# Kernel tuning notes

Measured on AMD Instinct MI355X. Metric: run time of the kernel, lower is better.

The kernel has to match this reference:

```python
import jax, jax.numpy as jnp
import numpy as np

N = 100000   # nodes
E = 1600000  # edges
D = 128      # feature dim (layers all 128)
G = 512      # graphs in batch
C = 10       # num_classes
EPS = 1e-5   # batchnorm eps


def setup_inputs() -> dict:
    key = jax.random.key(0)
    ks = jax.random.split(key, 16)
    s = 1.0 / np.sqrt(D)
    return {
        "x": jax.random.normal(ks[0], (N, D), jnp.float32),
        "edge_index": jax.random.randint(ks[1], (2, E), 0, N),
        "batch": jnp.sort(jax.random.randint(ks[2], (N,), 0, G)),
        "w1": jax.random.normal(ks[3], (D, D), jnp.float32) * s,
        "b1": jnp.zeros((D,), jnp.float32),
        "w2": jax.random.normal(ks[4], (D, D), jnp.float32) * s,
        "b2": jnp.zeros((D,), jnp.float32),
        "w3": jax.random.normal(ks[5], (D, D), jnp.float32) * s,
        "b3": jnp.zeros((D,), jnp.float32),
        "g1": jnp.ones((D,), jnp.float32),
        "be1": jnp.zeros((D,), jnp.float32),
        "g2": jnp.ones((D,), jnp.float32),
        "be2": jnp.zeros((D,), jnp.float32),
        "fc_w": jax.random.normal(ks[6], (D, C), jnp.float32) * s,
        "fc_b": jnp.zeros((C,), jnp.float32),
    }


def _gcn(x, src, dst, norm, W, b):
    # transform -> gather -> normalize -> scatter-add (PyG GCNConv)
    h = x @ W
    out = jax.ops.segment_sum(h[src] * norm[:, None], dst, num_segments=x.shape[0])
    return out + b


def _bn(x, g, b):
    # training-mode BatchNorm1d: batch mean / biased variance
    mu = jnp.mean(x, axis=0)
    var = jnp.mean((x - mu) ** 2, axis=0)
    return (x - mu) * jax.lax.rsqrt(var + EPS) * g + b


def reference(x, edge_index, batch, w1, b1, w2, b2, w3, b3, g1, be1, g2, be2, fc_w, fc_b):
    n = x.shape[0]
    loop = jnp.arange(n)
    src = jnp.concatenate([edge_index[0], loop])  # add self-loops
    dst = jnp.concatenate([edge_index[1], loop])
    deg = jax.ops.segment_sum(jnp.ones_like(src, x.dtype), dst, num_segments=n)
    dinv = jax.lax.rsqrt(jnp.maximum(deg, 1.0))  # deg >= 1 due to self-loops
    norm = dinv[src] * dinv[dst]  # symmetric normalization per edge

    h = jax.nn.relu(_gcn(x, src, dst, norm, w1, b1))        # conv1 + relu (bn1 unused, per source)
    h = jax.nn.relu(_gcn(h, src, dst, norm, w2, b2))        # conv2 + relu
    h = jax.nn.relu(_bn(h, g1, be1))                        # bn + relu
    h = jax.nn.relu(_gcn(h, src, dst, norm, w3, b3))        # conv3 + relu
    h = jax.nn.relu(_bn(h, g2, be2))                        # bn + relu

    cnt = jax.ops.segment_sum(jnp.ones((n,), h.dtype), batch, num_segments=G)
    pooled = jax.ops.segment_sum(h, batch, num_segments=G) / jnp.maximum(cnt, 1.0)[:, None]
    logits = pooled @ fc_w + fc_b
    return jax.nn.log_softmax(logits, axis=1)
```

## Files before the change

### kernel.cpp

```cpp
#include <hip/hip_runtime.h>
#include <hip/hip_bf16.h>
#include <math.h>

#define D 128
#define G_GRAPHS 512
#define C_CLASSES 10
#define BN_EPS 1e-5f
#define NBUCK_MAX 512
#define EDGE_CHUNK 4096
#define EPT 16

typedef unsigned short u16;
typedef unsigned int u32;
typedef unsigned short ushort4_t __attribute__((ext_vector_type(4)));
typedef unsigned short ushort8_t __attribute__((ext_vector_type(8)));
typedef __bf16 bf16x8 __attribute__((ext_vector_type(8)));
typedef float floatx4 __attribute__((ext_vector_type(4)));
union B8 { ushort8_t u; bf16x8 b; };

__device__ __forceinline__ float bf_lo(u32 v) { return __uint_as_float(v << 16); }
__device__ __forceinline__ float bf_hi(u32 v) { return __uint_as_float(v & 0xffff0000u); }
__device__ __forceinline__ u16 f2bf(float f) {
    union { float f; u32 u; } x; x.f = f;
    u32 r = x.u + 0x7fff + ((x.u >> 16) & 1);
    return (u16)(r >> 16);
}
__device__ __forceinline__ u32 pack2bf(float a, float b) {
    return (u32)f2bf(a) | ((u32)f2bf(b) << 16);
}


__global__ __launch_bounds__(256) void bucket_hist_kernel(
    const int* __restrict__ dst, int* __restrict__ bucketCnt, int E, int nbuck)
{
    __shared__ int h[NBUCK_MAX];
    int tid = threadIdx.x;
    for (int i = tid; i < NBUCK_MAX; i += 256) h[i] = 0;
    __syncthreads();
    for (int i = blockIdx.x * 256 + tid; i < E; i += gridDim.x * 256)
        atomicAdd(&h[dst[i] >> 8], 1);
    __syncthreads();
    for (int i = tid; i < nbuck; i += 256)
        if (h[i]) atomicAdd(&bucketCnt[i], h[i]);
}

__global__ void scan_buckets_kernel(
    const int* __restrict__ bucketCnt, int* __restrict__ bucketBase,
    int* __restrict__ bucketCursor, int* __restrict__ rowPtr, int nbuck, int N, int E)
{
    __shared__ int buf[2][512];
    int tid = threadIdx.x;
    int v = (tid < nbuck) ? bucketCnt[tid] : 0;
    buf[0][tid] = v;
    __syncthreads();
    int cur = 0;
    for (int off = 1; off < 512; off <<= 1) {
        buf[1 - cur][tid] = buf[cur][tid] + ((tid >= off) ? buf[cur][tid - off] : 0);
        cur ^= 1;
        __syncthreads();
    }
    if (tid < nbuck) {
        int b = buf[cur][tid] - v;
        bucketBase[tid] = b;
        bucketCursor[tid] = b;
    }
    if (tid == 0) { bucketBase[nbuck] = E; rowPtr[N] = E; }
}

__global__ __launch_bounds__(256) void scatter_pairs_kernel(
    const int* __restrict__ src, const int* __restrict__ dst,
    int* __restrict__ bucketCursor, u32* __restrict__ pairs, int E)
{
    __shared__ int h[NBUCK_MAX];
    __shared__ int base[NBUCK_MAX];
    int tid = threadIdx.x;
    int e0 = blockIdx.x * EDGE_CHUNK;
    for (int i = tid; i < NBUCK_MAX; i += 256) h[i] = 0;
    __syncthreads();
    int s[EPT], d[EPT], r[EPT];
#pragma unroll
    for (int j = 0; j < EPT; ++j) {
        int i = e0 + j * 256 + tid;
        if (i < E) {
            s[j] = src[i];
            d[j] = dst[i];
            r[j] = atomicAdd(&h[d[j] >> 8], 1);
        } else {
            d[j] = -1;
        }
    }
    __syncthreads();
    for (int i = tid; i < NBUCK_MAX; i += 256)
        if (h[i]) base[i] = atomicAdd(&bucketCursor[i], h[i]);
    __syncthreads();
#pragma unroll
    for (int j = 0; j < EPT; ++j) {
        if (d[j] >= 0) {
            int b = d[j] >> 8;
            pairs[base[b] + r[j]] = ((u32)s[j] << 8) | (u32)(d[j] & 255);
        }
    }
}

__global__ __launch_bounds__(256) void bucket_sort_kernel(
    const u32* __restrict__ pairs, const int* __restrict__ bucketBase,
    int* __restrict__ colIdx, int* __restrict__ rowPtr, float* __restrict__ dinv, int N)
{
    __shared__ int h[256];
    __shared__ int cur[256];
    __shared__ int sbuf[2][256];
    int tid = threadIdx.x;
    int b = blockIdx.x;
    int s = bucketBase[b], e = bucketBase[b + 1];
    h[tid] = 0;
    __syncthreads();
    for (int i = s + tid; i < e; i += 256)
        atomicAdd(&h[pairs[i] & 255], 1);
    __syncthreads();
    int cnt = h[tid];
    sbuf[0][tid] = cnt;
    __syncthreads();
    int c = 0;
    for (int off = 1; off < 256; off <<= 1) {
        sbuf[1 - c][tid] = sbuf[c][tid] + ((tid >= off) ? sbuf[c][tid - off] : 0);
        c ^= 1;
        __syncthreads();
    }
    int excl = sbuf[c][tid] - cnt;
    int v = b * 256 + tid;
    if (v < N) {
        rowPtr[v] = s + excl;
        dinv[v] = rsqrtf((float)(cnt + 1));
    }
    cur[tid] = s + excl;
    __syncthreads();
    for (int i = s + tid; i < e; i += 256) {
        u32 p = pairs[i];
        int pos = atomicAdd(&cur[p & 255], 1);
        colIdx[pos] = (int)(p >> 8);
    }
}

__global__ __launch_bounds__(256) void graph_bounds_kernel(
    const int* __restrict__ batch, int* __restrict__ gstart, int N)
{
    int i = blockIdx.x * 256 + threadIdx.x;
    if (i >= N) return;
    int b = batch[i];
    int prev = (i == 0) ? -1 : batch[i - 1];
    if (b != prev) {
        for (int g = prev + 1; g <= b; ++g) gstart[g] = i;
    }
    if (i == N - 1) {
        for (int g = b + 1; g <= G_GRAPHS; ++g) gstart[g] = N;
    }
}

__global__ __launch_bounds__(256) void wconv_kernel(
    const float4* __restrict__ w1, const float4* __restrict__ w2,
    const float4* __restrict__ w3, u16* __restrict__ wtAll, u32* __restrict__ tzero)
{
    int tid = threadIdx.x;
    if (blockIdx.x == 3) {
        if (tid < 64) tzero[tid] = 0;
        return;
    }
    const float4* W = (blockIdx.x == 0) ? w1 : (blockIdx.x == 1) ? w2 : w3;
    u16* Wt = wtAll + (size_t)blockIdx.x * D * D;
#pragma unroll
    for (int i = 0; i < 16; ++i) {
        int idx = tid + i * 256;
        int k = idx >> 5, c4 = idx & 31;
        float4 v = W[idx];
        Wt[(4 * c4 + 0) * D + k] = f2bf(v.x);
        Wt[(4 * c4 + 1) * D + k] = f2bf(v.y);
        Wt[(4 * c4 + 2) * D + k] = f2bf(v.z);
        Wt[(4 * c4 + 3) * D + k] = f2bf(v.w);
    }
}

#define XS_STRIDE 136
#define GEMM_GRID 768

__device__ __forceinline__ void gemm_core_and_store(
    const u16* Xs, const u16* Ws, const float* __restrict__ dinv,
    u16* __restrict__ Y, int row0, int nrows, int tid)
{
    int wid = tid >> 6, lane = tid & 63;
    int m = lane & 15, quad = lane >> 4;
    int xrow = wid * 16 + m;

    floatx4 acc[8] = {};
#pragma unroll
    for (int ks = 0; ks < 4; ++ks) {
        int kk = ks * 32 + quad * 8;
        B8 a;
        a.u = *(const ushort8_t*)&Xs[xrow * XS_STRIDE + kk];
#pragma unroll
        for (int t = 0; t < 8; ++t) {
            B8 b;
            b.u = *(const ushort8_t*)&Ws[(t * 16 + m) * XS_STRIDE + kk];
            acc[t] = __builtin_amdgcn_mfma_f32_16x16x32_bf16(b.b, a.b, acc[t], 0, 0, 0);
        }
    }
    int grow = row0 + xrow;
    if (grow < nrows) {
        float du = dinv[grow];
#pragma unroll
        for (int t = 0; t < 8; ++t) {
            ushort4_t o;
            o.x = f2bf(acc[t][0] * du); o.y = f2bf(acc[t][1] * du);
            o.z = f2bf(acc[t][2] * du); o.w = f2bf(acc[t][3] * du);
            *(ushort4_t*)&Y[(size_t)grow * D + t * 16 + quad * 4] = o;
        }
    }
}

__device__ __forceinline__ void stage_w(const u16* __restrict__ Wt, u16* Ws, int tid) {
    const ushort8_t* Wv = (const ushort8_t*)Wt;
#pragma unroll
    for (int i = 0; i < 8; ++i) {
        int idx = tid + i * 256;
        int n = idx >> 4, c8 = idx & 15;
        *(ushort8_t*)&Ws[n * XS_STRIDE + c8 * 8] = Wv[idx];
    }
}

__global__ __launch_bounds__(256) void gemm_mfma_f32in_kernel(
    const float4* __restrict__ X, const u16* __restrict__ Wt,
    const float* __restrict__ dinv, u16* __restrict__ Y, int nrows, int ntiles)
{
    __shared__ __align__(16) u16 Xs[64 * XS_STRIDE];
    __shared__ __align__(16) u16 Ws[128 * XS_STRIDE];
    int tid = threadIdx.x;
    stage_w(Wt, Ws, tid);
    for (int t = blockIdx.x; t < ntiles; t += gridDim.x) {
        int row0 = t * 64;
        __syncthreads();
#pragma unroll
        for (int i = 0; i < 8; ++i) {
            int idx = tid + i * 256;
            int r = idx >> 5, c4 = idx & 31;
            int gr = row0 + r;
            float4 v = make_float4(0.f, 0.f, 0.f, 0.f);
            if (gr < nrows) v = X[(size_t)gr * 32 + c4];
            ushort4_t o;
            o.x = f2bf(v.x); o.y = f2bf(v.y); o.z = f2bf(v.z); o.w = f2bf(v.w);
            *(ushort4_t*)&Xs[r * XS_STRIDE + c4 * 4] = o;
        }
        __syncthreads();
        gemm_core_and_store(Xs, Ws, dinv, Y, row0, nrows, tid);
    }
}

__global__ __launch_bounds__(256) void gemm_mfma_bf16in_kernel(
    const uint4* __restrict__ X, const u16* __restrict__ Wt,
    const float* __restrict__ gsum, const float* __restrict__ gsq,
    const float* __restrict__ gamma, const float* __restrict__ beta, float invN,
    const float* __restrict__ dinv, u16* __restrict__ Y, int nrows, int ntiles)
{
    __shared__ __align__(16) u16 Xs[64 * XS_STRIDE];
    __shared__ __align__(16) u16 Ws[128 * XS_STRIDE];
    __shared__ float scs[D], shs[D];
    int tid = threadIdx.x;
    bool fuse = (gsum != nullptr);
    stage_w(Wt, Ws, tid);
    if (fuse && tid < D) {
        float mu = gsum[tid] * invN;
        float var = gsq[tid] * invN - mu * mu;
        float sc = gamma[tid] * rsqrtf(var + BN_EPS);
        scs[tid] = sc;
        shs[tid] = beta[tid] - mu * sc;
    }
    for (int t = blockIdx.x; t < ntiles; t += gridDim.x) {
        int row0 = t * 64;
        __syncthreads();
#pragma unroll
        for (int i = 0; i < 4; ++i) {
            int idx = tid + i * 256;
            int r = idx >> 4, c8 = idx & 15;
            int gr = row0 + r;
            uint4 v = make_uint4(0, 0, 0, 0);
            if (gr < nrows) v = X[(size_t)gr * 16 + c8];
            if (fuse) {
                int k = c8 * 8;
                v.x = pack2bf(fmaxf(bf_lo(v.x) * scs[k]     + shs[k],     0.f),
                              fmaxf(bf_hi(v.x) * scs[k + 1] + shs[k + 1], 0.f));
                v.y = pack2bf(fmaxf(bf_lo(v.y) * scs[k + 2] + shs[k + 2], 0.f),
                              fmaxf(bf_hi(v.y) * scs[k + 3] + shs[k + 3], 0.f));
                v.z = pack2bf(fmaxf(bf_lo(v.z) * scs[k + 4] + shs[k + 4], 0.f),
                              fmaxf(bf_hi(v.z) * scs[k + 5] + shs[k + 5], 0.f));
                v.w = pack2bf(fmaxf(bf_lo(v.w) * scs[k + 6] + shs[k + 6], 0.f),
                              fmaxf(bf_hi(v.w) * scs[k + 7] + shs[k + 7], 0.f));
            }
            *(uint4*)&Xs[r * XS_STRIDE + c8 * 8] = v;
        }
        __syncthreads();
        gemm_core_and_store(Xs, Ws, dinv, Y, row0, nrows, tid);
    }
}

#define ACC8U(t)                                           \
    acc0 += bf_lo((t).x); acc1 += bf_hi((t).x);            \
    acc2 += bf_lo((t).y); acc3 += bf_hi((t).y);            \
    acc4 += bf_lo((t).z); acc5 += bf_hi((t).z);            \
    acc6 += bf_lo((t).w); acc7 += bf_hi((t).w);

__global__ __launch_bounds__(256) void aggregate_kernel(
    const uint4* __restrict__ T, const int* __restrict__ colIdx,
    const int* __restrict__ rowPtr, const float* __restrict__ dinv,
    const float* __restrict__ bias, u32* __restrict__ outH, int n, u32 zoff)
{
    int tid = threadIdx.x;
    int fg = tid & 15;
    int grp = tid >> 4;
    int row = blockIdx.x * 16 + grp;
    if (row >= n) return;

    const char* baseT = (const char*)T + fg * 16;

    uint4 sv = *(const uint4*)(baseT + ((size_t)(u32)row << 8));
    float acc0 = bf_lo(sv.x), acc1 = bf_hi(sv.x);
    float acc2 = bf_lo(sv.y), acc3 = bf_hi(sv.y);
    float acc4 = bf_lo(sv.z), acc5 = bf_hi(sv.z);
    float acc6 = bf_lo(sv.w), acc7 = bf_hi(sv.w);

    int s = rowPtr[row], e = rowPtr[row + 1];
    int len = e - s;
    const int* ci = colIdx + s;

    if (len > 0) {
        int nch = (len + 7) >> 3;
        u32 o0 = (u32)ci[0] << 8;
        u32 o1 = (1 < len) ? ((u32)ci[1] << 8) : zoff;
        u32 o2 = (2 < len) ? ((u32)ci[2] << 8) : zoff;
        u32 o3 = (3 < len) ? ((u32)ci[3] << 8) : zoff;
        u32 o4 = (4 < len) ? ((u32)ci[4] << 8) : zoff;
        u32 o5 = (5 < len) ? ((u32)ci[5] << 8) : zoff;
        u32 o6 = (6 < len) ? ((u32)ci[6] << 8) : zoff;
        u32 o7 = (7 < len) ? ((u32)ci[7] << 8) : zoff;
        uint4 t0 = *(const uint4*)(baseT + o0);
        uint4 t1 = *(const uint4*)(baseT + o1);
        uint4 t2 = *(const uint4*)(baseT + o2);
        uint4 t3 = *(const uint4*)(baseT + o3);
        uint4 t4 = *(const uint4*)(baseT + o4);
        uint4 t5 = *(const uint4*)(baseT + o5);
        uint4 t6 = *(const uint4*)(baseT + o6);
        uint4 t7 = *(const uint4*)(baseT + o7);
#pragma unroll 1
        for (int c = 1; c < nch; ++c) {
            int j = c * 8;
            int i0 = ci[j];     int i1 = ci[j + 1];
            int i2 = ci[j + 2]; int i3 = ci[j + 3];
            int i4 = ci[j + 4]; int i5 = ci[j + 5];
            int i6 = ci[j + 6]; int i7 = ci[j + 7];
            o0 = (j     < len) ? ((u32)i0 << 8) : zoff;
            o1 = (j + 1 < len) ? ((u32)i1 << 8) : zoff;
            o2 = (j + 2 < len) ? ((u32)i2 << 8) : zoff;
            o3 = (j + 3 < len) ? ((u32)i3 << 8) : zoff;
            o4 = (j + 4 < len) ? ((u32)i4 << 8) : zoff;
            o5 = (j + 5 < len) ? ((u32)i5 << 8) : zoff;
            o6 = (j + 6 < len) ? ((u32)i6 << 8) : zoff;
            o7 = (j + 7 < len) ? ((u32)i7 << 8) : zoff;
            ACC8U(t0); ACC8U(t1); ACC8U(t2); ACC8U(t3);
            ACC8U(t4); ACC8U(t5); ACC8U(t6); ACC8U(t7);
            t0 = *(const uint4*)(baseT + o0);
            t1 = *(const uint4*)(baseT + o1);
            t2 = *(const uint4*)(baseT + o2);
            t3 = *(const uint4*)(baseT + o3);
            t4 = *(const uint4*)(baseT + o4);
            t5 = *(const uint4*)(baseT + o5);
            t6 = *(const uint4*)(baseT + o6);
            t7 = *(const uint4*)(baseT + o7);
        }
        ACC8U(t0); ACC8U(t1); ACC8U(t2); ACC8U(t3);
        ACC8U(t4); ACC8U(t5); ACC8U(t6); ACC8U(t7);
    }

    float dr = dinv[row];
    const float2* bp = (const float2*)bias;
    float2 bq0 = bp[fg * 4 + 0];
    float2 bq1 = bp[fg * 4 + 1];
    float2 bq2 = bp[fg * 4 + 2];
    float2 bq3 = bp[fg * 4 + 3];
    uint4 o;
    o.x = pack2bf(fmaxf(dr * acc0 + bq0.x, 0.f), fmaxf(dr * acc1 + bq0.y, 0.f));
    o.y = pack2bf(fmaxf(dr * acc2 + bq1.x, 0.f), fmaxf(dr * acc3 + bq1.y, 0.f));
    o.z = pack2bf(fmaxf(dr * acc4 + bq2.x, 0.f), fmaxf(dr * acc5 + bq2.y, 0.f));
    o.w = pack2bf(fmaxf(dr * acc6 + bq3.x, 0.f), fmaxf(dr * acc7 + bq3.y, 0.f));
    *(uint4*)&outH[(size_t)row * 64 + fg * 4] = o;
}

__global__ __launch_bounds__(256) void bn_stats_kernel(
    const u32* __restrict__ H, int n, float* __restrict__ gsum, float* __restrict__ gsq)
{
    int tid = threadIdx.x;
    int c = tid & 63, rr = tid >> 6;
    float sA = 0.f, sA2 = 0.f, sB = 0.f, sB2 = 0.f;
    for (int row = blockIdx.x * 4 + rr; row < n; row += gridDim.x * 4) {
        u32 v = H[(size_t)row * 64 + c];
        float a = bf_lo(v), b = bf_hi(v);
        sA += a; sA2 += a * a; sB += b; sB2 += b * b;
    }
    __shared__ float shA[256], shA2[256], shB[256], shB2[256];
    shA[tid] = sA; shA2[tid] = sA2; shB[tid] = sB; shB2[tid] = sB2;
    __syncthreads();
    if (tid < 64) {
        float tA = shA[tid] + shA[tid + 64] + shA[tid + 128] + shA[tid + 192];
        float tA2 = shA2[tid] + shA2[tid + 64] + shA2[tid + 128] + shA2[tid + 192];
        float tB = shB[tid] + shB[tid + 64] + shB[tid + 128] + shB[tid + 192];
        float tB2 = shB2[tid] + shB2[tid + 64] + shB2[tid + 128] + shB2[tid + 192];
        atomicAdd(&gsum[2 * c], tA);
        atomicAdd(&gsq[2 * c], tA2);
        atomicAdd(&gsum[2 * c + 1], tB);
        atomicAdd(&gsq[2 * c + 1], tB2);
    }
}

__global__ __launch_bounds__(256) void pool_classify_kernel(
    const u32* __restrict__ H, const float* __restrict__ gsum, const float* __restrict__ gsq,
    const float* __restrict__ gamma, const float* __restrict__ beta, float invN,
    const int* __restrict__ gstart, const float* __restrict__ fcw,
    const float* __restrict__ fcb, float* __restrict__ out)
{
    int g = blockIdx.x;
    int tid = threadIdx.x;
    int c = tid & 63, q = tid >> 6;
    float muA = gsum[2 * c] * invN, muB = gsum[2 * c + 1] * invN;
    float vA = gsq[2 * c] * invN - muA * muA, vB = gsq[2 * c + 1] * invN - muB * muB;
    float scA = gamma[2 * c] * rsqrtf(vA + BN_EPS), scB = gamma[2 * c + 1] * rsqrtf(vB + BN_EPS);
    float shA = beta[2 * c] - muA * scA, shB = beta[2 * c + 1] - muB * scB;

    int s = gstart[g], cnt = gstart[g + 1] - s;
    float aA = 0.f, aB = 0.f;
    for (int i = q; i < cnt; i += 4) {
        u32 v = H[(size_t)(s + i) * 64 + c];
        aA += fmaxf(bf_lo(v) * scA + shA, 0.f);
        aB += fmaxf(bf_hi(v) * scB + shB, 0.f);
    }
    __shared__ float sA[256], sB[256];
    __shared__ float prow[D];
    __shared__ float lg[C_CLASSES];
    sA[tid] = aA; sB[tid] = aB;
    __syncthreads();
    if (tid < 64) {
        float tA = sA[tid] + sA[tid + 64] + sA[tid + 128] + sA[tid + 192];
        float tB = sB[tid] + sB[tid + 64] + sB[tid + 128] + sB[tid + 192];
        float inv = 1.f / (float)(cnt > 1 ? cnt : 1);
        prow[2 * tid] = tA * inv;
        prow[2 * tid + 1] = tB * inv;
    }
    __syncthreads();
    if (tid < C_CLASSES) {
        float sum = fcb[tid];
        for (int d = 0; d < D; ++d) sum += prow[d] * fcw[d * C_CLASSES + tid];
        lg[tid] = sum;
    }
    __syncthreads();
    if (tid == 0) {
        float mx = -1e30f;
        for (int k = 0; k < C_CLASSES; ++k) mx = fmaxf(mx, lg[k]);
        float se = 0.f;
        for (int k = 0; k < C_CLASSES; ++k) se += expf(lg[k] - mx);
        float lse = mx + logf(se);
        for (int k = 0; k < C_CLASSES; ++k) out[(size_t)g * C_CLASSES + k] = lg[k] - lse;
    }
}

extern "C" void kernel_launch(void* const* d_in, const int* in_sizes, int n_in,
                              void* d_out, int out_size, void* d_ws, size_t ws_size,
                              hipStream_t stream) {
    const float* x   = (const float*)d_in[0];
    const int* ei    = (const int*)d_in[1];
    const int* batch = (const int*)d_in[2];
    const float* w1  = (const float*)d_in[3];
    const float* b1  = (const float*)d_in[4];
    const float* w2  = (const float*)d_in[5];
    const float* b2  = (const float*)d_in[6];
    const float* w3  = (const float*)d_in[7];
    const float* b3  = (const float*)d_in[8];
    const float* g1  = (const float*)d_in[9];
    const float* be1 = (const float*)d_in[10];
    const float* g2  = (const float*)d_in[11];
    const float* be2 = (const float*)d_in[12];
    const float* fcw = (const float*)d_in[13];
    const float* fcb = (const float*)d_in[14];

    const int N = in_sizes[0] / D;
    const int E = in_sizes[1] / 2;
    const int* src = ei;
    const int* dst = ei + E;
    const int nbuck = (N + 255) >> 8;
    const float invN = 1.f / (float)N;

    char* p = (char*)d_ws;
    auto alloc = [&](size_t bytes) -> void* {
        void* r = (void*)p;
        p += (bytes + 255) & ~(size_t)255;
        return r;
    };
    int*   bucketCnt    = (int*)alloc(NBUCK_MAX * 4);
    float* statsacc     = (float*)alloc(4 * D * 4);
    float* gsum1 = statsacc, *gsq1 = statsacc + D, *gsum2 = statsacc + 2 * D, *gsq2 = statsacc + 3 * D;
    float* dinv     = (float*)alloc((size_t)N * 4);
    int*   rowPtr   = (int*)alloc((size_t)(N + 1) * 4);
    int*   colIdx   = (int*)alloc((size_t)E * 4);
    u32*   pairs    = (u32*)alloc((size_t)E * 4);
    int*   bucketBase   = (int*)alloc((NBUCK_MAX + 1) * 4);
    int*   bucketCursor = (int*)alloc(NBUCK_MAX * 4);
    int*   gstart  = (int*)alloc((G_GRAPHS + 1) * 4);
    u16*   wtAll   = (u16*)alloc((size_t)3 * D * D * 2);
    u16*   tmp     = (u16*)alloc((size_t)(N + 1) * D * 2);
    u16*   hbuf    = (u16*)alloc((size_t)N * D * 2);

    hipMemsetAsync(bucketCnt, 0, NBUCK_MAX * 4 + 4 * D * 4, stream);

    bucket_hist_kernel<<<512, 256, 0, stream>>>(dst, bucketCnt, E, nbuck);
    scan_buckets_kernel<<<1, 512, 0, stream>>>(bucketCnt, bucketBase, bucketCursor, rowPtr, nbuck, N, E);
    scatter_pairs_kernel<<<(E + EDGE_CHUNK - 1) / EDGE_CHUNK, 256, 0, stream>>>(src, dst, bucketCursor, pairs, E);
    bucket_sort_kernel<<<nbuck, 256, 0, stream>>>(pairs, bucketBase, colIdx, rowPtr, dinv, N);
    graph_bounds_kernel<<<(N + 255) / 256, 256, 0, stream>>>(batch, gstart, N);
    wconv_kernel<<<4, 256, 0, stream>>>((const float4*)w1, (const float4*)w2, (const float4*)w3,
                                        wtAll, (u32*)(tmp + (size_t)N * D));

    const int NT = (N + 63) / 64;
    const int GB = NT < GEMM_GRID ? NT : GEMM_GRID;
    const int AB = (N + 15) / 16;
    const u32 ZOFF = (u32)N << 8;

    gemm_mfma_f32in_kernel<<<GB, 256, 0, stream>>>((const float4*)x, wtAll, dinv, tmp, N, NT);
    aggregate_kernel<<<AB, 256, 0, stream>>>((const uint4*)tmp, colIdx, rowPtr, dinv, b1, (u32*)hbuf, N, ZOFF);
    gemm_mfma_bf16in_kernel<<<GB, 256, 0, stream>>>((const uint4*)hbuf, wtAll + D * D,
        nullptr, nullptr, nullptr, nullptr, 0.f, dinv, tmp, N, NT);
    aggregate_kernel<<<AB, 256, 0, stream>>>((const uint4*)tmp, colIdx, rowPtr, dinv, b2, (u32*)hbuf, N, ZOFF);
    bn_stats_kernel<<<1024, 256, 0, stream>>>((const u32*)hbuf, N, gsum1, gsq1);
    gemm_mfma_bf16in_kernel<<<GB, 256, 0, stream>>>((const uint4*)hbuf, wtAll + 2 * D * D,
        gsum1, gsq1, g1, be1, invN, dinv, tmp, N, NT);
    aggregate_kernel<<<AB, 256, 0, stream>>>((const uint4*)tmp, colIdx, rowPtr, dinv, b3, (u32*)hbuf, N, ZOFF);
    bn_stats_kernel<<<1024, 256, 0, stream>>>((const u32*)hbuf, N, gsum2, gsq2);
    pool_classify_kernel<<<G_GRAPHS, 256, 0, stream>>>((const u32*)hbuf, gsum2, gsq2, g2, be2, invN,
        gstart, fcw, fcb, (float*)d_out);
}
```

Measured before the change: 548.0 us.

## Sort aggregation rows by degree bucket and deepen gather pipeline to 16

Builds a degree histogram in the bucket sort, scans it in a spare wconv block, and scatters a node permutation so each aggregation block processes rows of similar degree, which reduces load imbalance between rows within a block. The aggregation loop now keeps two 8-wide gather batches in flight, processing 16 neighbors per iteration for more memory-level parallelism. The permutation adds a small kernel plus an indirection read, and output writes become scattered rather than contiguous. Random-graph degrees average about 16, so the degree buckets are coarse, and the deeper unroll increases register use.

```diff
diff --git a/kernel.cpp b/kernel.cpp
--- a/kernel.cpp
+++ b/kernel.cpp
@@ -104,7 +104,8 @@
 
 __global__ __launch_bounds__(256) void bucket_sort_kernel(
     const u32* __restrict__ pairs, const int* __restrict__ bucketBase,
-    int* __restrict__ colIdx, int* __restrict__ rowPtr, float* __restrict__ dinv, int N)
+    int* __restrict__ colIdx, int* __restrict__ rowPtr, float* __restrict__ dinv,
+    int* __restrict__ degHist, int N)
 {
     __shared__ int h[256];
     __shared__ int cur[256];
@@ -131,6 +132,9 @@
     if (v < N) {
         rowPtr[v] = s + excl;
         dinv[v] = rsqrtf((float)(cnt + 1));
+        int key = (cnt + 15) >> 4;
+        if (key > 15) key = 15;
+        atomicAdd(&degHist[key], 1);
     }
     cur[tid] = s + excl;
     __syncthreads();
@@ -158,11 +162,22 @@
 
 __global__ __launch_bounds__(256) void wconv_kernel(
     const float4* __restrict__ w1, const float4* __restrict__ w2,
-    const float4* __restrict__ w3, u16* __restrict__ wtAll, u32* __restrict__ tzero)
+    const float4* __restrict__ w3, u16* __restrict__ wtAll, u32* __restrict__ tzero,
+    const int* __restrict__ degHist, int* __restrict__ degCursor)
 {
     int tid = threadIdx.x;
     if (blockIdx.x == 3) {
         if (tid < 64) tzero[tid] = 0;
+        return;
+    }
+    if (blockIdx.x == 4) {
+        if (tid == 0) {
+            int base = 0;
+            for (int k = 15; k >= 0; --k) {
+                degCursor[k] = base;
+                base += degHist[k];
+            }
+        }
         return;
     }
     const float4* W = (blockIdx.x == 0) ? w1 : (blockIdx.x == 1) ? w2 : w3;
@@ -177,6 +192,29 @@
         Wt[(4 * c4 + 2) * D + k] = f2bf(v.z);
         Wt[(4 * c4 + 3) * D + k] = f2bf(v.w);
     }
+}
+
+__global__ __launch_bounds__(256) void perm_scatter_kernel(
+    const int* __restrict__ rowPtr, int* __restrict__ degCursor,
+    int* __restrict__ perm, int N)
+{
+    __shared__ int lh[16], lbase[16];
+    int tid = threadIdx.x;
+    if (tid < 16) lh[tid] = 0;
+    __syncthreads();
+    int v = blockIdx.x * 256 + tid;
+    int key = 0, r = 0;
+    bool ok = (v < N);
+    if (ok) {
+        int deg = rowPtr[v + 1] - rowPtr[v];
+        key = (deg + 15) >> 4;
+        if (key > 15) key = 15;
+        r = atomicAdd(&lh[key], 1);
+    }
+    __syncthreads();
+    if (tid < 16 && lh[tid] > 0) lbase[tid] = atomicAdd(&degCursor[tid], lh[tid]);
+    __syncthreads();
+    if (ok) perm[lbase[key] + r] = v;
 }
 
 #define XS_STRIDE 136
@@ -306,16 +344,48 @@
     acc4 += bf_lo((t).z); acc5 += bf_hi((t).z);            \
     acc6 += bf_lo((t).w); acc7 += bf_hi((t).w);
 
+#define IDX8(i, jj)                                        \
+    i##0 = ci[(jj)];     i##1 = ci[(jj) + 1];              \
+    i##2 = ci[(jj) + 2]; i##3 = ci[(jj) + 3];              \
+    i##4 = ci[(jj) + 4]; i##5 = ci[(jj) + 5];              \
+    i##6 = ci[(jj) + 6]; i##7 = ci[(jj) + 7];
+
+#define OFF8(o, i, jj)                                     \
+    o##0 = ((jj)     < len) ? ((u32)i##0 << 8) : zoff;     \
+    o##1 = ((jj) + 1 < len) ? ((u32)i##1 << 8) : zoff;     \
+    o##2 = ((jj) + 2 < len) ? ((u32)i##2 << 8) : zoff;     \
+    o##3 = ((jj) + 3 < len) ? ((u32)i##3 << 8) : zoff;     \
+    o##4 = ((jj) + 4 < len) ? ((u32)i##4 << 8) : zoff;     \
+    o##5 = ((jj) + 5 < len) ? ((u32)i##5 << 8) : zoff;     \
+    o##6 = ((jj) + 6 < len) ? ((u32)i##6 << 8) : zoff;     \
+    o##7 = ((jj) + 7 < len) ? ((u32)i##7 << 8) : zoff;
+
+#define GAT8(t, o)                                         \
+    t##0 = *(const uint4*)(baseT + o##0);                  \
+    t##1 = *(const uint4*)(baseT + o##1);                  \
+    t##2 = *(const uint4*)(baseT + o##2);                  \
+    t##3 = *(const uint4*)(baseT + o##3);                  \
+    t##4 = *(const uint4*)(baseT + o##4);                  \
+    t##5 = *(const uint4*)(baseT + o##5);                  \
+    t##6 = *(const uint4*)(baseT + o##6);                  \
+    t##7 = *(const uint4*)(baseT + o##7);
+
+#define ACCC(t)                                            \
+    ACC8U(t##0); ACC8U(t##1); ACC8U(t##2); ACC8U(t##3);    \
+    ACC8U(t##4); ACC8U(t##5); ACC8U(t##6); ACC8U(t##7);
+
 __global__ __launch_bounds__(256) void aggregate_kernel(
     const uint4* __restrict__ T, const int* __restrict__ colIdx,
     const int* __restrict__ rowPtr, const float* __restrict__ dinv,
-    const float* __restrict__ bias, u32* __restrict__ outH, int n, u32 zoff)
+    const float* __restrict__ bias, const int* __restrict__ perm,
+    u32* __restrict__ outH, int n, u32 zoff)
 {
     int tid = threadIdx.x;
     int fg = tid & 15;
     int grp = tid >> 4;
-    int row = blockIdx.x * 16 + grp;
-    if (row >= n) return;
+    int slot = blockIdx.x * 16 + grp;
+    if (slot >= n) return;
+    int row = perm[slot];
 
     const char* baseT = (const char*)T + fg * 16;
 
@@ -330,51 +400,34 @@
     const int* ci = colIdx + s;
 
     if (len > 0) {
-        int nch = (len + 7) >> 3;
-        u32 o0 = (u32)ci[0] << 8;
-        u32 o1 = (1 < len) ? ((u32)ci[1] << 8) : zoff;
-        u32 o2 = (2 < len) ? ((u32)ci[2] << 8) : zoff;
-        u32 o3 = (3 < len) ? ((u32)ci[3] << 8) : zoff;
-        u32 o4 = (4 < len) ? ((u32)ci[4] << 8) : zoff;
-        u32 o5 = (5 < len) ? ((u32)ci[5] << 8) : zoff;
-        u32 o6 = (6 < len) ? ((u32)ci[6] << 8) : zoff;
-        u32 o7 = (7 < len) ? ((u32)ci[7] << 8) : zoff;
-        uint4 t0 = *(const uint4*)(baseT + o0);
-        uint4 t1 = *(const uint4*)(baseT + o1);
-        uint4 t2 = *(const uint4*)(baseT + o2);
-        uint4 t3 = *(const uint4*)(baseT + o3);
-        uint4 t4 = *(const uint4*)(baseT + o4);
-        uint4 t5 = *(const uint4*)(baseT + o5);
-        uint4 t6 = *(const uint4*)(baseT + o6);
-        uint4 t7 = *(const uint4*)(baseT + o7);
+        int npairs = (len + 15) >> 4;
+        int ia0, ia1, ia2, ia3, ia4, ia5, ia6, ia7;
+        int ib0, ib1, ib2, ib3, ib4, ib5, ib6, ib7;
+        u32 oa0, oa1, oa2, oa3, oa4, oa5, oa6, oa7;
+        u32 ob0, ob1, ob2, ob3, ob4, ob5, ob6, ob7;
+        uint4 t0, t1, t2, t3, t4, t5, t6, t7;
+        uint4 u0, u1, u2, u3, u4, u5, u6, u7;
+
+        IDX8(ia, 0); IDX8(ib, 8);
+        OFF8(oa, ia, 0);
+        GAT8(t, oa);
+        OFF8(ob, ib, 8);
+        IDX8(ia, 16);
+        GAT8(u, ob);
+
 #pragma unroll 1
-        for (int c = 1; c < nch; ++c) {
-            int j = c * 8;
-            int i0 = ci[j];     int i1 = ci[j + 1];
-            int i2 = ci[j + 2]; int i3 = ci[j + 3];
-            int i4 = ci[j + 4]; int i5 = ci[j + 5];
-            int i6 = ci[j + 6]; int i7 = ci[j + 7];
-            o0 = (j     < len) ? ((u32)i0 << 8) : zoff;
-            o1 = (j + 1 < len) ? ((u32)i1 << 8) : zoff;
-            o2 = (j + 2 < len) ? ((u32)i2 << 8) : zoff;
-            o3 = (j + 3 < len) ? ((u32)i3 << 8) : zoff;
-            o4 = (j + 4 < len) ? ((u32)i4 << 8) : zoff;
-            o5 = (j + 5 < len) ? ((u32)i5 << 8) : zoff;
-            o6 = (j + 6 < len) ? ((u32)i6 << 8) : zoff;
-            o7 = (j + 7 < len) ? ((u32)i7 << 8) : zoff;
-            ACC8U(t0); ACC8U(t1); ACC8U(t2); ACC8U(t3);
-            ACC8U(t4); ACC8U(t5); ACC8U(t6); ACC8U(t7);
-            t0 = *(const uint4*)(baseT + o0);
-            t1 = *(const uint4*)(baseT + o1);
-            t2 = *(const uint4*)(baseT + o2);
-            t3 = *(const uint4*)(baseT + o3);
-            t4 = *(const uint4*)(baseT + o4);
-            t5 = *(const uint4*)(baseT + o5);
-            t6 = *(const uint4*)(baseT + o6);
-            t7 = *(const uint4*)(baseT + o7);
-        }
-        ACC8U(t0); ACC8U(t1); ACC8U(t2); ACC8U(t3);
-        ACC8U(t4); ACC8U(t5); ACC8U(t6); ACC8U(t7);
+        for (int p = 1; p < npairs; ++p) {
+            int j = p << 4;
+            OFF8(oa, ia, j);
+            IDX8(ib, j + 8);
+            ACCC(t);
+            GAT8(t, oa);
+            OFF8(ob, ib, j + 8);
+            ACCC(u);
+            IDX8(ia, j + 16);
+            GAT8(u, ob);
+        }
+        ACCC(t); ACCC(u);
     }
 
     float dr = dinv[row];
@@ -502,6 +555,8 @@
     int*   bucketCnt    = (int*)alloc(NBUCK_MAX * 4);
     float* statsacc     = (float*)alloc(4 * D * 4);
     float* gsum1 = statsacc, *gsq1 = statsacc + D, *gsum2 = statsacc + 2 * D, *gsq2 = statsacc + 3 * D;
+    int*   degHist      = (int*)alloc(32 * 4);
+    int*   degCursor    = degHist + 16;
     float* dinv     = (float*)alloc((size_t)N * 4);
     int*   rowPtr   = (int*)alloc((size_t)(N + 1) * 4);
     int*   colIdx   = (int*)alloc((size_t)E * 4);
@@ -509,19 +564,21 @@
     int*   bucketBase   = (int*)alloc((NBUCK_MAX + 1) * 4);
     int*   bucketCursor = (int*)alloc(NBUCK_MAX * 4);
     int*   gstart  = (int*)alloc((G_GRAPHS + 1) * 4);
+    int*   perm    = (int*)alloc((size_t)N * 4);
     u16*   wtAll   = (u16*)alloc((size_t)3 * D * D * 2);
     u16*   tmp     = (u16*)alloc((size_t)(N + 1) * D * 2);
     u16*   hbuf    = (u16*)alloc((size_t)N * D * 2);
 
-    hipMemsetAsync(bucketCnt, 0, NBUCK_MAX * 4 + 4 * D * 4, stream);
+    hipMemsetAsync(bucketCnt, 0, NBUCK_MAX * 4 + 4 * D * 4 + 32 * 4, stream);
 
     bucket_hist_kernel<<<512, 256, 0, stream>>>(dst, bucketCnt, E, nbuck);
     scan_buckets_kernel<<<1, 512, 0, stream>>>(bucketCnt, bucketBase, bucketCursor, rowPtr, nbuck, N, E);
     scatter_pairs_kernel<<<(E + EDGE_CHUNK - 1) / EDGE_CHUNK, 256, 0, stream>>>(src, dst, bucketCursor, pairs, E);
-    bucket_sort_kernel<<<nbuck, 256, 0, stream>>>(pairs, bucketBase, colIdx, rowPtr, dinv, N);
+    bucket_sort_kernel<<<nbuck, 256, 0, stream>>>(pairs, bucketBase, colIdx, rowPtr, dinv, degHist, N);
     graph_bounds_kernel<<<(N + 255) / 256, 256, 0, stream>>>(batch, gstart, N);
-    wconv_kernel<<<4, 256, 0, stream>>>((const float4*)w1, (const float4*)w2, (const float4*)w3,
-                                        wtAll, (u32*)(tmp + (size_t)N * D));
+    wconv_kernel<<<5, 256, 0, stream>>>((const float4*)w1, (const float4*)w2, (const float4*)w3,
+                                        wtAll, (u32*)(tmp + (size_t)N * D), degHist, degCursor);
+    perm_scatter_kernel<<<(N + 255) / 256, 256, 0, stream>>>(rowPtr, degCursor, perm, N);
 
     const int NT = (N + 63) / 64;
     const int GB = NT < GEMM_GRID ? NT : GEMM_GRID;
@@ -529,14 +586,14 @@
     const u32 ZOFF = (u32)N << 8;
 
     gemm_mfma_f32in_kernel<<<GB, 256, 0, stream>>>((const float4*)x, wtAll, dinv, tmp, N, NT);
-    aggregate_kernel<<<AB, 256, 0, stream>>>((const uint4*)tmp, colIdx, rowPtr, dinv, b1, (u32*)hbuf, N, ZOFF);
+    aggregate_kernel<<<AB, 256, 0, stream>>>((const uint4*)tmp, colIdx, rowPtr, dinv, b1, perm, (u32*)hbuf, N, ZOFF);
     gemm_mfma_bf16in_kernel<<<GB, 256, 0, stream>>>((const uint4*)hbuf, wtAll + D * D,
         nullptr, nullptr, nullptr, nullptr, 0.f, dinv, tmp, N, NT);
-    aggregate_kernel<<<AB, 256, 0, stream>>>((const uint4*)tmp, colIdx, rowPtr, dinv, b2, (u32*)hbuf, N, ZOFF);
+    aggregate_kernel<<<AB, 256, 0, stream>>>((const uint4*)tmp, colIdx, rowPtr, dinv, b2, perm, (u32*)hbuf, N, ZOFF);
     bn_stats_kernel<<<1024, 256, 0, stream>>>((const u32*)hbuf, N, gsum1, gsq1);
     gemm_mfma_bf16in_kernel<<<GB, 256, 0, stream>>>((const uint4*)hbuf, wtAll + 2 * D * D,
         gsum1, gsq1, g1, be1, invN, dinv, tmp, N, NT);
-    aggregate_kernel<<<AB, 256, 0, stream>>>((const uint4*)tmp, colIdx, rowPtr, dinv, b3, (u32*)hbuf, N, ZOFF);
+    aggregate_kernel<<<AB, 256, 0, stream>>>((const uint4*)tmp, colIdx, rowPtr, dinv, b3, perm, (u32*)hbuf, N, ZOFF);
     bn_stats_kernel<<<1024, 256, 0, stream>>>((const u32*)hbuf, N, gsum2, gsq2);
     pool_classify_kernel<<<G_GRAPHS, 256, 0, stream>>>((const u32*)hbuf, gsum2, gsq2, g2, be2, invN,
         gstart, fcw, fcb, (float*)d_out);
```

Result: slower. 1.320 ms (+140.9%).
